# Kernel tuning notes

Measured on AMD Instinct MI355X. Metric: run time of the kernel, lower is better.

## Reference

```python
import jax, jax.numpy as jnp
import numpy as np

B, S, E, P, H, F = 4, 4096, 256, 32, 8, 1024
DH = E // H
LN_EPS = 1e-5


def setup_inputs() -> dict:
    key = jax.random.key(0)
    ks = jax.random.split(key, 12)
    dt = jnp.float32
    return {
        "src": jax.random.normal(ks[0], (B, S, E), dt),
        "pos_embed": jax.random.normal(ks[1], (B, P, S), dt),
        # learnable positional transform (pos_linear: P -> P)
        "Wpos": jax.random.normal(ks[2], (P, P), dt) * (1.0 / np.sqrt(P)),
        "bpos": jnp.zeros((P,), dt),
        # RBF kernel hyperparameters (ScaleKernel(RBFKernel)) -- positive scalars
        "lengthscale": jnp.full((), 2.0, dt),
        "outputscale": jnp.full((), 1.0, dt),
        # value / output projections of multihead attention
        "Wv": jax.random.normal(ks[3], (E, E), dt) * (1.0 / np.sqrt(E)),
        "bv": jnp.zeros((E,), dt),
        "Wo": jax.random.normal(ks[4], (E, E), dt) * (1.0 / np.sqrt(E)),
        "bo": jnp.zeros((E,), dt),
        # feed-forward
        "W1": jax.random.normal(ks[5], (F, E), dt) * (1.0 / np.sqrt(E)),
        "b1": jnp.zeros((F,), dt),
        "W2": jax.random.normal(ks[6], (E, F), dt) * (1.0 / np.sqrt(F)),
        "b2": jnp.zeros((E,), dt),
        # layer norms
        "ln1_g": jnp.ones((E,), dt), "ln1_b": jnp.zeros((E,), dt),
        "ln2_g": jnp.ones((E,), dt), "ln2_b": jnp.zeros((E,), dt),
    }


def _layer_norm(x, g, b):
    mu = jnp.mean(x, -1, keepdims=True)
    var = jnp.mean(jnp.square(x - mu), -1, keepdims=True)
    return (x - mu) * jax.lax.rsqrt(var + LN_EPS) * g + b


def _rbf_scores(x, lengthscale, outputscale):
    # x: [B, S, P] -> scaled RBF kernel matrix [B, S, S]
    xs = x / lengthscale
    sq = jnp.sum(xs * xs, axis=-1)  # [B, S]
    d2 = sq[:, :, None] + sq[:, None, :] - 2.0 * jnp.einsum('bsp,btp->bst', xs, xs)
    d2 = jnp.maximum(d2, 0.0)
    return outputscale * jnp.exp(-0.5 * d2)


def reference(src, pos_embed, Wpos, bpos, lengthscale, outputscale,
              Wv, bv, Wo, bo, W1, b1, W2, b2, ln1_g, ln1_b, ln2_g, ln2_b):
    b, s, e = src.shape
    # learnable positional transform: [B,P,S] -> [B,S,P] -> linear -> back
    pe = jnp.einsum('bps,op->bos', pos_embed, Wpos) + bpos[None, :, None]  # [B,P,S]
    # GP-kernel attention scores over sequence positions
    scores = _rbf_scores(pe.transpose(0, 2, 1), lengthscale, outputscale)  # [B,S,S]
    attn = jax.nn.softmax(scores, axis=-1)
    # value projection, per-head weighted sum (scores shared across heads)
    v = (src @ Wv.T + bv).reshape(b, s, H, DH)
    ctx = jnp.einsum('bqk,bkhd->bqhd', attn, v).reshape(b, s, e)
    attn_out = ctx @ Wo.T + bo
    x = _layer_norm(src + attn_out, ln1_g, ln1_b)
    ff = jax.nn.relu(x @ W1.T + b1) @ W2.T + b2
    return _layer_norm(x + ff, ln2_g, ln2_b)
```

## Files before the change

### kernel.cpp

```cpp
#include <hip/hip_runtime.h>
#include <stdint.h>

#define BN 4
#define SN 4096
#define EN 256
#define PN 32
#define FN 1024
#define BS (BN*SN)
#define PAUG 64

typedef uint16_t bf16_t;
typedef short v4s  __attribute__((ext_vector_type(4)));
typedef short v8s  __attribute__((ext_vector_type(8)));
typedef __bf16 bf16x8 __attribute__((ext_vector_type(8)));
typedef float v4f   __attribute__((ext_vector_type(4)));
typedef float v16f  __attribute__((ext_vector_type(16)));

#define MFMA16(a,b,c) __builtin_amdgcn_mfma_f32_16x16x32_bf16(a,b,c,0,0,0)
#define MFMA32(a,b,c) __builtin_amdgcn_mfma_f32_32x32x16_bf16(a,b,c,0,0,0)

__device__ __forceinline__ float b2f(bf16_t x){
    uint32_t u = ((uint32_t)x) << 16; float f; __builtin_memcpy(&f, &u, 4); return f;
}
__device__ __forceinline__ bf16_t f2b(float f){
    uint32_t u; __builtin_memcpy(&u, &f, 4);
    u += 0x7FFFu + ((u >> 16) & 1u);
    return (bf16_t)(u >> 16);
}
__device__ __forceinline__ bf16x8 ldb8(const bf16_t* p){
    v8s r = *(const v8s*)p; return __builtin_bit_cast(bf16x8, r);
}
__device__ __forceinline__ bf16x8 ldb8u(const bf16_t* p){
    v4s lo = *(const v4s*)p;
    v4s hi = *(const v4s*)(p + 4);
    v8s r = __builtin_shufflevector(lo, hi, 0,1,2,3,4,5,6,7);
    return __builtin_bit_cast(bf16x8, r);
}
__device__ __forceinline__ float ldsc(const float* p){ return *p; }
__device__ __forceinline__ float ldsc(const bf16_t* p){ return b2f(*p); }
__device__ __forceinline__ void stsc(float* p, float v){ *p = v; }
__device__ __forceinline__ void stsc(bf16_t* p, float v){ *p = f2b(v); }

#if __has_builtin(__builtin_amdgcn_exp2f)
__device__ __forceinline__ float fexp2(float x){ return __builtin_amdgcn_exp2f(x); }
#else
__device__ __forceinline__ float fexp2(float x){ return exp2f(x); }
#endif

#if __has_builtin(__builtin_amdgcn_cvt_pk_bf16_f32)
typedef __bf16 bf16x2 __attribute__((ext_vector_type(2)));
__device__ __forceinline__ uint32_t pkbf16(float a, float b){
    bf16x2 r = __builtin_amdgcn_cvt_pk_bf16_f32(a, b);
    return __builtin_bit_cast(uint32_t, r);
}
#else
__device__ __forceinline__ uint32_t pkbf16(float a, float b){
    return (uint32_t)f2b(a) | ((uint32_t)f2b(b) << 16);
}
#endif

typedef const __attribute__((address_space(1))) uint32_t* glds_gp;
typedef __attribute__((address_space(3))) uint32_t* glds_lp;
__device__ __forceinline__ void glds16(const bf16_t* g, bf16_t* l){
    __builtin_amdgcn_global_load_lds((glds_gp)g, (glds_lp)l, 16, 0, 0);
}

__global__ __launch_bounds__(256) void prep_kernel(
    const float* __restrict__ src, bf16_t* __restrict__ srcb,
    const float* __restrict__ Wv, bf16_t* __restrict__ Wvb,
    const float* __restrict__ Wo, bf16_t* __restrict__ Wob,
    const float* __restrict__ W1, bf16_t* __restrict__ W1b,
    const float* __restrict__ W2, bf16_t* __restrict__ W2b,
    const float* __restrict__ pos, const float* __restrict__ Wp,
    const float* __restrict__ bp,  const float* __restrict__ lsp,
    bf16_t* __restrict__ xk, bf16_t* __restrict__ xq)
{
    __shared__ float Wsh[PN*PN];
    __shared__ float bsh[PN];
    int bid = blockIdx.x;
    int tid = threadIdx.x;

    if (bid < 4736){
        const float* sp; bf16_t* dp; int off;
        if (bid < 4096){ sp = src; dp = srcb; off = (bid*256 + tid)*4; }
        else {
            int i = ((bid - 4096)*256 + tid)*4;
            if      (i <  65536){ sp=Wv; dp=Wvb; off=i; }
            else if (i < 131072){
                int idx = i - 65536;
                float4 f = *(const float4*)(Wo + idx);
                v4s o;
                o.x = (short)f2b(f.x); o.y = (short)f2b(f.y);
                o.z = (short)f2b(f.z); o.w = (short)f2b(f.w);
                int n = idx >> 8, k = idx & 255;
                int dst = (((n>>4)*8 + (k>>5))*64 + (((k>>3)&3)*16 + (n&15)))*8 + (k&7);
                *(v4s*)(Wob + dst) = o;
                return;
            }
            else if (i < 393216){ sp=W1; dp=W1b; off=i-131072; }
            else                { sp=W2; dp=W2b; off=i-393216; }
        }
        float4 f = *(const float4*)(sp + off);
        v4s o;
        o.x = (short)f2b(f.x); o.y = (short)f2b(f.y);
        o.z = (short)f2b(f.z); o.w = (short)f2b(f.w);
        *(v4s*)(dp + off) = o;
        return;
    }

    int pb = bid - 4736;
    int b  = pb >> 4;
    int s  = (pb & 15)*256 + tid;

    for (int i = tid; i < PN*PN; i += 256) Wsh[i] = Wp[i];
    if (tid < PN) bsh[tid] = bp[tid];
    __syncthreads();

    float inv_ls = 1.0f / lsp[0];
    const float c1f = 1.4426950408889634f;

    float col[PN];
    #pragma unroll
    for (int p = 0; p < PN; p++) col[p] = pos[((size_t)b*PN + p)*SN + s];

    uint16_t xb[PN], qb[PN];
    float sq = 0.f;
    #pragma unroll 4
    for (int o = 0; o < PN; o++){
        float pe = bsh[o];
        #pragma unroll
        for (int p = 0; p < PN; p++) pe += col[p] * Wsh[o*PN + p];
        float pv = pe * inv_ls;
        uint16_t h = f2b(pv);
        xb[o] = h;
        qb[o] = f2b(c1f * pv);
        float xr = b2f(h);
        sq += xr * xr;
    }

    size_t base = ((size_t)b*SN + s) * PAUG;
    v8s pk[8];
    #pragma unroll
    for (int c = 0; c < 4; c++)
        #pragma unroll
        for (int j = 0; j < 8; j++) ((short*)&pk[c])[j] = (short)xb[c*8 + j];
    #pragma unroll
    for (int c = 4; c < 8; c++)
        #pragma unroll
        for (int j = 0; j < 8; j++) ((short*)&pk[c])[j] = 0;
    ((short*)&pk[4])[0] = (short)f2b(-0.5f * sq);
    ((short*)&pk[4])[1] = (short)0x3F80;
    #pragma unroll
    for (int c = 0; c < 8; c++) *(v8s*)(xk + base + c*8) = pk[c];

    #pragma unroll
    for (int c = 0; c < 4; c++)
        #pragma unroll
        for (int j = 0; j < 8; j++) ((short*)&pk[c])[j] = (short)qb[c*8 + j];
    ((short*)&pk[4])[0] = (short)f2b(c1f);
    ((short*)&pk[4])[1] = (short)f2b(-0.5f * sq * c1f);
    #pragma unroll
    for (int c = 0; c < 8; c++) *(v8s*)(xq + base + c*8) = pk[c];
}

template<int EPI, typename OutT>
__global__ __launch_bounds__(256) void gemm_t(
    const bf16_t* __restrict__ A, const bf16_t* __restrict__ W,
    const float* __restrict__ bias, OutT* __restrict__ out,
    bf16_t* __restrict__ vt, int N, int K)
{
    __shared__ __align__(16) bf16_t At[2][4096];
    __shared__ __align__(16) bf16_t Wt[2][4096];
    int tid = threadIdx.x;
    int lane = tid & 63, wv = tid >> 6, col = lane & 15, quad = lane >> 4;
    int m0 = blockIdx.x * 64, n0 = blockIdx.y * 64;
    int nck = K >> 6;

    int srow = tid >> 3;
    int spc  = (tid & 7) ^ (srow & 7);
    const bf16_t* asrc = A + (size_t)(m0 + srow)*K + spc*8;
    const bf16_t* wsrc = W + (size_t)(n0 + srow)*K + spc*8;

    v4f acc[4];
    #pragma unroll
    for (int t = 0; t < 4; t++) acc[t] = (v4f){0.f,0.f,0.f,0.f};

    glds16(asrc, &At[0][tid*8]);
    glds16(asrc + (size_t)32*K, &At[0][2048 + tid*8]);
    glds16(wsrc, &Wt[0][tid*8]);
    glds16(wsrc + (size_t)32*K, &Wt[0][2048 + tid*8]);
    __syncthreads();

    for (int c = 0; c < nck; c++){
        int cb = c & 1;
        if (c + 1 < nck){
            glds16(asrc + (c+1)*64, &At[cb^1][tid*8]);
            glds16(asrc + (size_t)32*K + (c+1)*64, &At[cb^1][2048 + tid*8]);
            glds16(wsrc + (c+1)*64, &Wt[cb^1][tid*8]);
            glds16(wsrc + (size_t)32*K + (c+1)*64, &Wt[cb^1][2048 + tid*8]);
        }
        #pragma unroll
        for (int kc = 0; kc < 2; kc++){
            int pc = ((kc*4 + quad) ^ (col & 7)) * 8;
            bf16x8 a = ldb8(&At[cb][(wv*16 + col)*64 + pc]);
            #pragma unroll
            for (int t = 0; t < 4; t++){
                bf16x8 b = ldb8(&Wt[cb][(t*16 + col)*64 + pc]);
                acc[t] = MFMA16(a, b, acc[t]);
            }
        }
        __syncthreads();
    }

    float bfv[4];
    #pragma unroll
    for (int t = 0; t < 4; t++) bfv[t] = bias[n0 + t*16 + col];

    if constexpr (EPI == 3){
        __shared__ uint16_t Tsh[64*74];
        #pragma unroll
        for (int r = 0; r < 4; r++)
            #pragma unroll
            for (int t = 0; t < 4; t++)
                Tsh[(wv*16 + quad*4 + r)*74 + t*16 + col] = f2b(acc[t][r] + bfv[t]);
        __syncthreads();
        int e = tid & 63, sc = tid >> 6;
        int b = m0 >> 12;
        int sbat = m0 & (SN-1);
        int eb   = (n0 + e) >> 5;
        int l31e = (n0 + e) & 31;
        int k16  = (sbat >> 4) + sc;
        v8s p0, p1;
        #pragma unroll
        for (int i = 0; i < 8; i++) ((short*)&p0)[i] = (short)Tsh[(sc*16 + i)*74 + e];
        #pragma unroll
        for (int i = 0; i < 8; i++) ((short*)&p1)[i] = (short)Tsh[(sc*16 + 8 + i)*74 + e];
        bf16_t* dst = vt + ((((size_t)b*8 + eb)*256 + k16)*64 + l31e)*8;
        *(v8s*)dst = p0;
        *(v8s*)(dst + 256) = p1;
    } else {
        #pragma unroll
        for (int r = 0; r < 4; r++){
            int row = m0 + wv*16 + quad*4 + r;
            #pragma unroll
            for (int t = 0; t < 4; t++){
                float y = acc[t][r] + bfv[t];
                if constexpr (EPI == 1) y = fmaxf(y, 0.f);
                stsc(out + (size_t)row*N + n0 + t*16 + col, y);
            }
        }
    }
}

__global__ __launch_bounds__(512, 4) void ffn_ln_kernel(
    const bf16_t* __restrict__ x,  const bf16_t* __restrict__ W1b,
    const float* __restrict__ b1,  const bf16_t* __restrict__ W2b,
    const float* __restrict__ b2,  const float* __restrict__ gamma,
    const float* __restrict__ beta, float* __restrict__ out)
{
    __shared__ __align__(16) bf16_t W1c[16384];
    __shared__ __align__(16) bf16_t W2c[16384];
    __shared__ __align__(16) bf16_t Hs[32*68];
    __shared__ float b1sh[1024];
    __shared__ float lnb[4][32][2];

    int tid  = threadIdx.x;
    int lane = tid & 63;
    int wv   = tid >> 6;
    int col  = lane & 15;
    int quad = lane >> 4;
    int mw   = wv >> 2;
    int nw   = wv & 3;
    int m0   = blockIdx.x * 32;

    b1sh[tid]       = b1[tid];
    b1sh[512 + tid] = b1[512 + tid];

    const bf16_t* xrow = x + (size_t)(m0 + mw*16 + col)*EN + quad*8;
    bf16x8 xr[8];
    #pragma unroll
    for (int kk = 0; kk < 8; kk++) xr[kk] = ldb8(xrow + kk*32);

    float b2v[4], gv[4], bev[4];
    #pragma unroll
    for (int t2 = 0; t2 < 4; t2++){
        int nn = nw*64 + t2*16 + col;
        b2v[t2] = b2[nn]; gv[t2] = gamma[nn]; bev[t2] = beta[nn];
    }

    v4f acc[4];
    #pragma unroll
    for (int t2 = 0; t2 < 4; t2++) acc[t2] = (v4f){0.f,0.f,0.f,0.f};

    int wr  = tid >> 3;
    int pp  = tid & 7;
    int swz = (pp ^ (wr & 7)) * 8;

    #pragma unroll 1
    for (int c = 0; c < 16; c++){
        #pragma unroll
        for (int s = 0; s < 4; s++)
            glds16(W1b + (size_t)(c*64 + wr)*256 + s*64 + swz,
                   &W1c[s*4096 + tid*8]);
        #pragma unroll
        for (int s2 = 0; s2 < 4; s2++)
            glds16(W2b + (size_t)(s2*64 + wr)*1024 + c*64 + swz,
                   &W2c[s2*4096 + tid*8]);
        asm volatile("s_waitcnt vmcnt(0)" ::: "memory");
        __builtin_amdgcn_s_barrier();
        __builtin_amdgcn_sched_barrier(0);

        int hl = nw*16 + col;
        v4f hacc = (v4f){0.f,0.f,0.f,0.f};
        #pragma unroll
        for (int kk = 0; kk < 8; kk++){
            bf16x8 b = ldb8(&W1c[(kk>>1)*4096 + hl*64
                             + ((((kk&1)*4 + quad) ^ (hl & 7))*8)]);
            hacc = MFMA16(xr[kk], b, hacc);
        }
        float bb = b1sh[c*64 + hl];
        #pragma unroll
        for (int r = 0; r < 4; r++)
            Hs[(mw*16 + quad*4 + r)*68 + hl] = f2b(fmaxf(hacc[r] + bb, 0.f));
        asm volatile("s_waitcnt lgkmcnt(0)" ::: "memory");
        __builtin_amdgcn_s_barrier();
        __builtin_amdgcn_sched_barrier(0);

        #pragma unroll
        for (int kk2 = 0; kk2 < 2; kk2++){
            bf16x8 a2 = ldb8u(&Hs[(mw*16 + col)*68 + kk2*32 + quad*8]);
            #pragma unroll
            for (int t2 = 0; t2 < 4; t2++){
                int nn = nw*64 + t2*16 + col;
                bf16x8 bfr = ldb8(&W2c[(nn>>6)*4096 + (nn&63)*64
                                  + (((kk2*4 + quad) ^ (col & 7))*8)]);
                acc[t2] = MFMA16(a2, bfr, acc[t2]);
            }
        }
        asm volatile("s_waitcnt lgkmcnt(0)" ::: "memory");
        __builtin_amdgcn_s_barrier();
    }

    float v[4][4];
    float s1[4], s2[4];
    #pragma unroll
    for (int r = 0; r < 4; r++){ s1[r] = 0.f; s2[r] = 0.f; }
    #pragma unroll
    for (int r = 0; r < 4; r++){
        int row = m0 + mw*16 + quad*4 + r;
        #pragma unroll
        for (int t2 = 0; t2 < 4; t2++){
            int nn = nw*64 + t2*16 + col;
            float xv = acc[t2][r] + b2v[t2] + b2f(x[(size_t)row*EN + nn]);
            v[t2][r] = xv; s1[r] += xv; s2[r] += xv*xv;
        }
    }
    #pragma unroll
    for (int r = 0; r < 4; r++){
        #pragma unroll
        for (int m = 1; m <= 8; m <<= 1){
            s1[r] += __shfl_xor(s1[r], m);
            s2[r] += __shfl_xor(s2[r], m);
        }
    }
    if (col == 0){
        #pragma unroll
        for (int r = 0; r < 4; r++){
            int rl = mw*16 + quad*4 + r;
            lnb[nw][rl][0] = s1[r];
            lnb[nw][rl][1] = s2[r];
        }
    }
    __syncthreads();
    #pragma unroll
    for (int r = 0; r < 4; r++){
        int rl  = mw*16 + quad*4 + r;
        int row = m0 + rl;
        float S1 = lnb[0][rl][0] + lnb[1][rl][0] + lnb[2][rl][0] + lnb[3][rl][0];
        float S2 = lnb[0][rl][1] + lnb[1][rl][1] + lnb[2][rl][1] + lnb[3][rl][1];
        float mu = S1 * (1.f/256.f);
        float rs = rsqrtf(S2 * (1.f/256.f) - mu*mu + 1e-5f);
        #pragma unroll
        for (int t2 = 0; t2 < 4; t2++){
            int nn = nw*64 + t2*16 + col;
            out[(size_t)row*EN + nn] = (v[t2][r] - mu)*rs*gv[t2] + bev[t2];
        }
    }
}

__global__ __launch_bounds__(512, 2) void attn_kernel(
    const bf16_t* __restrict__ xk, const bf16_t* __restrict__ xq,
    const bf16_t* __restrict__ vf, const float* __restrict__ osp,
    const bf16_t* __restrict__ wof, const float* __restrict__ bo,
    const bf16_t* __restrict__ res, const float* __restrict__ gamma,
    const float* __restrict__ beta, bf16_t* __restrict__ out)
{
    __shared__ __align__(16) bf16_t Wtb[2][64*260];
    __shared__ __align__(16) bf16_t Qs[64*64];
    __shared__ __align__(16) bf16_t Osh[64*256];
    __shared__ float densh[8][64];
    __shared__ float dent[64];
    __shared__ float lnw[8][64][2];

    int tid  = threadIdx.x;
    int lane = tid & 63;
    int wv   = tid >> 6;
    int col  = lane & 15;
    int quad = lane >> 4;
    int l31  = lane & 31;
    int half = lane >> 5;

    int bid = blockIdx.x;
    int b   = (bid & 7) >> 1;
    int qi  = ((bid >> 3) << 1) | (bid & 1);
    int q0  = qi * 64;

    float k2 = 1.4426950408889634f * osp[0];

    const bf16_t* xkb = xk + (size_t)b * SN * PAUG;
    const bf16_t* xqb = xq + (size_t)b * SN * PAUG;
    const bf16_t* vfb = vf + (((size_t)b*8 + wv)*256)*512 + lane*8;

    {
        int qrow = tid >> 3;
        int qpc  = (tid & 7) ^ (qrow & 7);
        glds16(xqb + (size_t)(q0 + qrow)*PAUG + qpc*8, &Qs[tid*8]);
    }

    v16f acc[2];
    #pragma unroll
    for (int qg = 0; qg < 2; qg++)
        #pragma unroll
        for (int i = 0; i < 16; i++) acc[qg][i] = 0.f;
    float den[4] = {0.f, 0.f, 0.f, 0.f};
    const v4f zero = (v4f){0.f,0.f,0.f,0.f};

    bf16x8 kf[2][2];
    #pragma unroll
    for (int kg = 0; kg < 2; kg++)
        #pragma unroll
        for (int h = 0; h < 2; h++)
            kf[kg][h] = ldb8(xkb + (size_t)(wv*32 + kg*16 + col)*PAUG + h*32 + quad*8);

    __syncthreads();

    for (int c = 0; c < 16; c++){
        int cb = c & 1;
        bf16x8 vr[16];
        #pragma unroll
        for (int sk = 0; sk < 16; sk++)
            vr[sk] = ldb8(vfb + (size_t)(c*16 + sk)*512);

        #pragma unroll
        for (int qg = 0; qg < 2; qg++){
            #pragma unroll
            for (int g2 = 0; g2 < 2; g2++){
                int qr = qg*32 + g2*16 + col;
                bf16x8 qa = ldb8(&Qs[qr*64 + ((quad    ) ^ (col & 7))*8]);
                bf16x8 qb = ldb8(&Qs[qr*64 + ((4 + quad) ^ (col & 7))*8]);
                #pragma unroll
                for (int kg = 0; kg < 2; kg++){
                    v4f st = MFMA16(kf[kg][0], qa, zero);
                    st = MFMA16(kf[kg][1], qb, st);
                    #pragma unroll
                    for (int rp = 0; rp < 2; rp++){
                        float w0 = fexp2(fmaf(k2, fexp2(st[rp*2+0]), -k2));
                        float w1 = fexp2(fmaf(k2, fexp2(st[rp*2+1]), -k2));
                        den[qg*2+g2] += w0 + w1;
                        *(uint32_t*)&Wtb[cb][qr*260 + wv*32 + kg*16 + quad*4 + rp*2]
                            = pkbf16(w0, w1);
                    }
                }
            }
        }

        if (c + 1 < 16){
            #pragma unroll
            for (int kg = 0; kg < 2; kg++)
                #pragma unroll
                for (int h = 0; h < 2; h++)
                    kf[kg][h] = ldb8(xkb + (size_t)((c+1)*256 + wv*32 + kg*16 + col)*PAUG
                                     + h*32 + quad*8);
        }

        asm volatile("s_waitcnt lgkmcnt(0)" ::: "memory");
        __builtin_amdgcn_s_barrier();
        __builtin_amdgcn_sched_barrier(0);

        #pragma unroll
        for (int qg = 0; qg < 2; qg++){
            #pragma unroll
            for (int sk4 = 0; sk4 < 4; sk4++){
                bf16x8 af[4];
                #pragma unroll
                for (int j = 0; j < 4; j++)
                    af[j] = ldb8u(&Wtb[cb][(qg*32 + l31)*260 + (sk4*4 + j)*16 + half*8]);
                #pragma unroll
                for (int j = 0; j < 4; j++)
                    acc[qg] = MFMA32(af[j], vr[sk4*4 + j], acc[qg]);
            }
        }
    }

    bf16x8 wf0[8];
    #pragma unroll
    for (int kc = 0; kc < 8; kc++)
        wf0[kc] = ldb8(wof + (size_t)(((wv*2+0)*8 + kc)*64 + lane)*8);

    #pragma unroll
    for (int d = 0; d < 4; d++){
        den[d] += __shfl_xor(den[d], 16);
        den[d] += __shfl_xor(den[d], 32);
    }
    if (lane < 16){
        #pragma unroll
        for (int qg = 0; qg < 2; qg++)
            #pragma unroll
            for (int g2 = 0; g2 < 2; g2++)
                densh[wv][qg*32 + g2*16 + lane] = den[qg*2+g2];
    }
    __syncthreads();
    if (tid < 64){
        float s = 0.f;
        #pragma unroll
        for (int w = 0; w < 8; w++) s += densh[w][tid];
        dent[tid] = 1.f / s;
    }
    __syncthreads();

    #pragma unroll
    for (int qg = 0; qg < 2; qg++){
        #pragma unroll
        for (int rg = 0; rg < 16; rg++){
            int qrow = qg*32 + (rg & 3) + 8*(rg >> 2) + 4*half;
            int e = wv*32 + l31;
            int g = e >> 3;
            Osh[qrow*256 + ((g ^ (qrow & 7))*8) + (e & 7)] = f2b(acc[qg][rg] * dent[qrow]);
        }
    }
    __syncthreads();

    v4f y[4][2];
    #pragma unroll
    for (int qg = 0; qg < 4; qg++)
        #pragma unroll
        for (int t = 0; t < 2; t++) y[qg][t] = (v4f){0.f,0.f,0.f,0.f};

    #pragma unroll
    for (int kc = 0; kc < 8; kc++){
        bf16x8 b1 = ldb8(wof + (size_t)(((wv*2+1)*8 + kc)*64 + lane)*8);
        #pragma unroll
        for (int qg = 0; qg < 4; qg++){
            bf16x8 a = ldb8(&Osh[(qg*16 + col)*256 + (((kc*4 + quad) ^ (col & 7))*8)]);
            y[qg][0] = MFMA16(a, wf0[kc], y[qg][0]);
            y[qg][1] = MFMA16(a, b1, y[qg][1]);
        }
    }

    size_t growb = (size_t)b*SN + q0;
    float bo0 = bo[wv*32 + col], bo1 = bo[wv*32 + 16 + col];
    #pragma unroll
    for (int qg = 0; qg < 4; qg++){
        #pragma unroll
        for (int r = 0; r < 4; r++){
            int row = qg*16 + quad*4 + r;
            float x0 = y[qg][0][r] + bo0 + b2f(res[(growb + row)*EN + wv*32 + col]);
            float x1 = y[qg][1][r] + bo1 + b2f(res[(growb + row)*EN + wv*32 + 16 + col]);
            y[qg][0][r] = x0; y[qg][1][r] = x1;
            float s1 = x0 + x1, s2 = x0*x0 + x1*x1;
            #pragma unroll
            for (int m = 1; m <= 8; m <<= 1){
                s1 += __shfl_xor(s1, m);
                s2 += __shfl_xor(s2, m);
            }
            if (col == 0){
                lnw[wv][row][0] = s1;
                lnw[wv][row][1] = s2;
            }
        }
    }
    __syncthreads();

    float g0 = gamma[wv*32 + col],      g1v = gamma[wv*32 + 16 + col];
    float e0 = beta[wv*32 + col],       e1v = beta[wv*32 + 16 + col];
    #pragma unroll
    for (int qg = 0; qg < 4; qg++){
        #pragma unroll
        for (int r = 0; r < 4; r++){
            int row = qg*16 + quad*4 + r;
            float S1 = 0.f, S2 = 0.f;
            #pragma unroll
            for (int w = 0; w < 8; w++){ S1 += lnw[w][row][0]; S2 += lnw[w][row][1]; }
            float mu = S1 * (1.f/256.f);
            float rs = rsqrtf(S2 * (1.f/256.f) - mu*mu + 1e-5f);
            out[(growb + row)*EN + wv*32 + col]      = f2b((y[qg][0][r]-mu)*rs*g0 + e0);
            out[(growb + row)*EN + wv*32 + 16 + col] = f2b((y[qg][1][r]-mu)*rs*g1v + e1v);
        }
    }
}

extern "C" void kernel_launch(void* const* d_in, const int* in_sizes, int n_in,
                              void* d_out, int out_size, void* d_ws, size_t ws_size,
                              hipStream_t stream)
{
    (void)in_sizes; (void)n_in; (void)out_size; (void)ws_size;
    const float* src  = (const float*)d_in[0];
    const float* pos  = (const float*)d_in[1];
    const float* Wpos = (const float*)d_in[2];
    const float* bpos = (const float*)d_in[3];
    const float* ls   = (const float*)d_in[4];
    const float* os   = (const float*)d_in[5];
    const float* Wv   = (const float*)d_in[6];
    const float* bv   = (const float*)d_in[7];
    const float* Wo   = (const float*)d_in[8];
    const float* bo   = (const float*)d_in[9];
    const float* W1   = (const float*)d_in[10];
    const float* b1   = (const float*)d_in[11];
    const float* W2   = (const float*)d_in[12];
    const float* b2   = (const float*)d_in[13];
    const float* g1   = (const float*)d_in[14];
    const float* be1  = (const float*)d_in[15];
    const float* g2   = (const float*)d_in[16];
    const float* be2  = (const float*)d_in[17];

    char* w = (char*)d_ws;
    bf16_t* xkb  = (bf16_t*)(w);
    bf16_t* xqb  = (bf16_t*)(w + ( 2u<<20));
    bf16_t* Wvb  = (bf16_t*)(w + ( 4u<<20));
    bf16_t* Wob  = (bf16_t*)(w + ( 4u<<20) + (1u<<18));
    bf16_t* W1b  = (bf16_t*)(w + ( 5u<<20));
    bf16_t* W2b  = (bf16_t*)(w + ( 6u<<20));
    bf16_t* srcb = (bf16_t*)(w + ( 8u<<20));
    bf16_t* vtg  = (bf16_t*)(w + (16u<<20));
    bf16_t* xws  = (bf16_t*)(w + (24u<<20));

    prep_kernel<<<dim3(4800), 256, 0, stream>>>(
        src, srcb, Wv, Wvb, Wo, Wob, W1, W1b, W2, W2b,
        pos, Wpos, bpos, ls, xkb, xqb);

    gemm_t<3, bf16_t><<<dim3(BS/64, EN/64), 256, 0, stream>>>(
        srcb, Wvb, bv, (bf16_t*)nullptr, vtg, EN, EN);
    attn_kernel<<<dim3(256), 512, 0, stream>>>(
        xkb, xqb, vtg, os, Wob, bo, srcb, g1, be1, xws);
    ffn_ln_kernel<<<dim3(BS/32), 512, 0, stream>>>(
        xws, W1b, b1, W2b, b2, g2, be2, (float*)d_out);
}
```

Measured before the change: 226.3 us.

## Warp-specialize attention: 4 waves compute RBF weights, 4 waves do PV MFMAs

Splits the 8 waves of the attention block into producers, which compute the scores, exp weights and denominators for a 256-key chunk into a double-buffered LDS tile, and consumers, which run the weight-times-V MFMAs for the previous chunk. Each consumer wave now covers 64 output columns with two accumulator sets and two V register arrays. The aim is to overlap exp-heavy VALU work with the MFMA work across waves instead of running them in sequence in every wave. In exchange, each wave does twice the per-chunk work of its role, consumer register pressure roughly doubles (occupancy may fall), and the loop gains one extra pipeline iteration.

After: 412.4 us. +82.2%, slower.

```diff
diff --git a/kernel.cpp b/kernel.cpp
--- a/kernel.cpp
+++ b/kernel.cpp
@@ -398,7 +398,7 @@
     __shared__ __align__(16) bf16_t Wtb[2][64*260];
     __shared__ __align__(16) bf16_t Qs[64*64];
     __shared__ __align__(16) bf16_t Osh[64*256];
-    __shared__ float densh[8][64];
+    __shared__ float densh[4][64];
     __shared__ float dent[64];
     __shared__ float lnw[8][64][2];
 
@@ -409,6 +409,7 @@
     int quad = lane >> 4;
     int l31  = lane & 31;
     int half = lane >> 5;
+    int sub  = wv & 3;
 
     int bid = blockIdx.x;
     int b   = (bid & 7) >> 1;
@@ -419,7 +420,8 @@
 
     const bf16_t* xkb = xk + (size_t)b * SN * PAUG;
     const bf16_t* xqb = xq + (size_t)b * SN * PAUG;
-    const bf16_t* vfb = vf + (((size_t)b*8 + wv)*256)*512 + lane*8;
+    const bf16_t* vfb0 = vf + (((size_t)b*8 + sub*2 + 0)*256)*512 + lane*8;
+    const bf16_t* vfb1 = vf + (((size_t)b*8 + sub*2 + 1)*256)*512 + lane*8;
 
     {
         int qrow = tid >> 3;
@@ -427,79 +429,92 @@
         glds16(xqb + (size_t)(q0 + qrow)*PAUG + qpc*8, &Qs[tid*8]);
     }
 
-    v16f acc[2];
-    #pragma unroll
-    for (int qg = 0; qg < 2; qg++)
-        #pragma unroll
-        for (int i = 0; i < 16; i++) acc[qg][i] = 0.f;
+    v16f acc[2][2];
+    #pragma unroll
+    for (int eg = 0; eg < 2; eg++)
+        #pragma unroll
+        for (int qg = 0; qg < 2; qg++)
+            #pragma unroll
+            for (int i = 0; i < 16; i++) acc[eg][qg][i] = 0.f;
+    bf16x8 vrA[16], vrB[16];
     float den[4] = {0.f, 0.f, 0.f, 0.f};
     const v4f zero = (v4f){0.f,0.f,0.f,0.f};
 
-    bf16x8 kf[2][2];
-    #pragma unroll
-    for (int kg = 0; kg < 2; kg++)
-        #pragma unroll
-        for (int h = 0; h < 2; h++)
-            kf[kg][h] = ldb8(xkb + (size_t)(wv*32 + kg*16 + col)*PAUG + h*32 + quad*8);
-
-    __syncthreads();
-
-    for (int c = 0; c < 16; c++){
-        int cb = c & 1;
-        bf16x8 vr[16];
-        #pragma unroll
-        for (int sk = 0; sk < 16; sk++)
-            vr[sk] = ldb8(vfb + (size_t)(c*16 + sk)*512);
-
-        #pragma unroll
-        for (int qg = 0; qg < 2; qg++){
-            #pragma unroll
-            for (int g2 = 0; g2 < 2; g2++){
-                int qr = qg*32 + g2*16 + col;
-                bf16x8 qa = ldb8(&Qs[qr*64 + ((quad    ) ^ (col & 7))*8]);
-                bf16x8 qb = ldb8(&Qs[qr*64 + ((4 + quad) ^ (col & 7))*8]);
+    __syncthreads();
+
+    #pragma unroll 1
+    for (int it = 0; it <= 16; it++){
+        if (wv < 4){
+            if (it < 16){
+                int cb = it & 1;
                 #pragma unroll
-                for (int kg = 0; kg < 2; kg++){
-                    v4f st = MFMA16(kf[kg][0], qa, zero);
-                    st = MFMA16(kf[kg][1], qb, st);
+                for (int hh = 0; hh < 2; hh++){
+                    bf16x8 kfh[2][2];
                     #pragma unroll
-                    for (int rp = 0; rp < 2; rp++){
-                        float w0 = fexp2(fmaf(k2, fexp2(st[rp*2+0]), -k2));
-                        float w1 = fexp2(fmaf(k2, fexp2(st[rp*2+1]), -k2));
-                        den[qg*2+g2] += w0 + w1;
-                        *(uint32_t*)&Wtb[cb][qr*260 + wv*32 + kg*16 + quad*4 + rp*2]
-                            = pkbf16(w0, w1);
+                    for (int kg2 = 0; kg2 < 2; kg2++){
+                        const bf16_t* kr = xkb
+                            + (size_t)(it*256 + sub*64 + (hh*2 + kg2)*16 + col)*PAUG
+                            + quad*8;
+                        kfh[kg2][0] = ldb8(kr);
+                        kfh[kg2][1] = ldb8(kr + 32);
+                    }
+                    #pragma unroll
+                    for (int qg = 0; qg < 2; qg++){
+                        #pragma unroll
+                        for (int g2 = 0; g2 < 2; g2++){
+                            int qr = qg*32 + g2*16 + col;
+                            bf16x8 qa = ldb8(&Qs[qr*64 + ((quad    ) ^ (col & 7))*8]);
+                            bf16x8 qb = ldb8(&Qs[qr*64 + ((4 + quad) ^ (col & 7))*8]);
+                            #pragma unroll
+                            for (int kg2 = 0; kg2 < 2; kg2++){
+                                v4f st = MFMA16(kfh[kg2][0], qa, zero);
+                                st = MFMA16(kfh[kg2][1], qb, st);
+                                #pragma unroll
+                                for (int rp = 0; rp < 2; rp++){
+                                    float w0 = fexp2(fmaf(k2, fexp2(st[rp*2+0]), -k2));
+                                    float w1 = fexp2(fmaf(k2, fexp2(st[rp*2+1]), -k2));
+                                    den[qg*2+g2] += w0 + w1;
+                                    *(uint32_t*)&Wtb[cb][qr*260 + sub*64
+                                        + (hh*2+kg2)*16 + quad*4 + rp*2]
+                                        = pkbf16(w0, w1);
+                                }
+                            }
+                        }
                     }
                 }
             }
-        }
-
-        if (c + 1 < 16){
-            #pragma unroll
-            for (int kg = 0; kg < 2; kg++)
+        } else {
+            if (it >= 1){
+                int par = (it - 1) & 1;
                 #pragma unroll
-                for (int h = 0; h < 2; h++)
-                    kf[kg][h] = ldb8(xkb + (size_t)((c+1)*256 + wv*32 + kg*16 + col)*PAUG
-                                     + h*32 + quad*8);
-        }
-
+                for (int qg = 0; qg < 2; qg++){
+                    #pragma unroll
+                    for (int sk4 = 0; sk4 < 4; sk4++){
+                        bf16x8 af[4];
+                        #pragma unroll
+                        for (int j = 0; j < 4; j++)
+                            af[j] = ldb8u(&Wtb[par][(qg*32 + l31)*260
+                                          + (sk4*4 + j)*16 + half*8]);
+                        #pragma unroll
+                        for (int j = 0; j < 4; j++){
+                            acc[0][qg] = MFMA32(af[j], vrA[sk4*4 + j], acc[0][qg]);
+                            acc[1][qg] = MFMA32(af[j], vrB[sk4*4 + j], acc[1][qg]);
+                        }
+                    }
+                }
+            }
+            if (it < 16){
+                #pragma unroll
+                for (int sk = 0; sk < 16; sk++)
+                    vrA[sk] = ldb8(vfb0 + (size_t)(it*16 + sk)*512);
+                #pragma unroll
+                for (int sk = 0; sk < 16; sk++)
+                    vrB[sk] = ldb8(vfb1 + (size_t)(it*16 + sk)*512);
+            }
+        }
         asm volatile("s_waitcnt lgkmcnt(0)" ::: "memory");
         __builtin_amdgcn_s_barrier();
         __builtin_amdgcn_sched_barrier(0);
-
-        #pragma unroll
-        for (int qg = 0; qg < 2; qg++){
-            #pragma unroll
-            for (int sk4 = 0; sk4 < 4; sk4++){
-                bf16x8 af[4];
-                #pragma unroll
-                for (int j = 0; j < 4; j++)
-                    af[j] = ldb8u(&Wtb[cb][(qg*32 + l31)*260 + (sk4*4 + j)*16 + half*8]);
-                #pragma unroll
-                for (int j = 0; j < 4; j++)
-                    acc[qg] = MFMA32(af[j], vr[sk4*4 + j], acc[qg]);
-            }
-        }
     }
 
     bf16x8 wf0[8];
@@ -512,7 +527,7 @@
         den[d] += __shfl_xor(den[d], 16);
         den[d] += __shfl_xor(den[d], 32);
     }
-    if (lane < 16){
+    if (wv < 4 && lane < 16){
         #pragma unroll
         for (int qg = 0; qg < 2; qg++)
             #pragma unroll
@@ -521,21 +536,25 @@
     }
     __syncthreads();
     if (tid < 64){
-        float s = 0.f;
-        #pragma unroll
-        for (int w = 0; w < 8; w++) s += densh[w][tid];
+        float s = densh[0][tid] + densh[1][tid] + densh[2][tid] + densh[3][tid];
         dent[tid] = 1.f / s;
     }
     __syncthreads();
 
-    #pragma unroll
-    for (int qg = 0; qg < 2; qg++){
-        #pragma unroll
-        for (int rg = 0; rg < 16; rg++){
-            int qrow = qg*32 + (rg & 3) + 8*(rg >> 2) + 4*half;
-            int e = wv*32 + l31;
-            int g = e >> 3;
-            Osh[qrow*256 + ((g ^ (qrow & 7))*8) + (e & 7)] = f2b(acc[qg][rg] * dent[qrow]);
+    if (wv >= 4){
+        #pragma unroll
+        for (int eg = 0; eg < 2; eg++){
+            #pragma unroll
+            for (int qg = 0; qg < 2; qg++){
+                #pragma unroll
+                for (int rg = 0; rg < 16; rg++){
+                    int qrow = qg*32 + (rg & 3) + 8*(rg >> 2) + 4*half;
+                    int e = sub*64 + eg*32 + l31;
+                    int g = e >> 3;
+                    Osh[qrow*256 + ((g ^ (qrow & 7))*8) + (e & 7)]
+                        = f2b(acc[eg][qg][rg] * dent[qrow]);
+                }
+            }
         }
     }
     __syncthreads();
```
